# Kernel tuning notes

Hardware: AMD Instinct MI355X
Metric: run time of the kernel (lower is better)

The kernel has to match this reference:

```python
import jax, jax.numpy as jnp
import numpy as np

EMB = 1024
HEADS = 16
HEAD_SZ = EMB // HEADS
EPS = 1e-5


def _layernorm(x, g, b):
    mu = jnp.mean(x, axis=-1, keepdims=True)
    var = jnp.mean(jnp.square(x - mu), axis=-1, keepdims=True)
    return (x - mu) * jax.lax.rsqrt(var + EPS) * g + b


def setup_inputs() -> dict:
    key = jax.random.key(0)
    ks = jax.random.split(key, 12)
    s_in = 1.0 / np.sqrt(EMB)
    s_h = 1.0 / np.sqrt(4 * EMB)
    return {
        "x": jax.random.normal(ks[0], (4, 1024, EMB), jnp.float32),
        # per-head Q/K/V projections stacked: [H, EMB, HEAD_SZ], no bias
        "wq": jax.random.normal(ks[1], (HEADS, EMB, HEAD_SZ), jnp.float32) * s_in,
        "wk": jax.random.normal(ks[2], (HEADS, EMB, HEAD_SZ), jnp.float32) * s_in,
        "wv": jax.random.normal(ks[3], (HEADS, EMB, HEAD_SZ), jnp.float32) * s_in,
        "w_proj": jax.random.normal(ks[4], (EMB, EMB), jnp.float32) * s_in,
        "b_proj": jnp.zeros((EMB,), jnp.float32),
        "w1": jax.random.normal(ks[5], (EMB, 4 * EMB), jnp.float32) * s_in,
        "b1": jnp.zeros((4 * EMB,), jnp.float32),
        "w2": jax.random.normal(ks[6], (4 * EMB, EMB), jnp.float32) * s_h,
        "b2": jnp.zeros((EMB,), jnp.float32),
        "g1": jnp.ones((EMB,), jnp.float32),
        "be1": jnp.zeros((EMB,), jnp.float32),
        "g2": jnp.ones((EMB,), jnp.float32),
        "be2": jnp.zeros((EMB,), jnp.float32),
    }


def reference(x, wq, wk, wv, w_proj, b_proj, w1, b1, w2, b2, g1, be1, g2, be2):
    B, T, C = x.shape
    # --- self-attention (pre-norm) ---
    h = _layernorm(x, g1, be1)
    q = jnp.einsum("btc,hcd->bhtd", h, wq)
    k = jnp.einsum("btc,hcd->bhtd", h, wk)
    v = jnp.einsum("btc,hcd->bhtd", h, wv)
    scale = 1.0 / jnp.sqrt(jnp.asarray(HEAD_SZ, x.dtype))
    scores = jnp.einsum("bhtd,bhsd->bhts", q, k) * scale  # non-causal: SDPA called with no mask
    attn = jax.nn.softmax(scores, axis=-1)
    o = jnp.einsum("bhts,bhsd->bhtd", attn, v)
    o = o.transpose(0, 2, 1, 3).reshape(B, T, C)  # concat heads (same order as torch.cat)
    sa_out = o @ w_proj + b_proj
    x = x + sa_out
    # --- feed-forward; note ln2 applied twice, faithful to source ---
    t = _layernorm(x, g2, be2)
    t = _layernorm(t, g2, be2)
    ff = jax.nn.relu(t @ w1 + b1) @ w2 + b2
    return x + ff
```

## Files before the change

### kernel.cpp

```cpp
#include <hip/hip_runtime.h>
#include <hip/hip_bf16.h>
#include <math.h>
#include <stdint.h>

typedef __bf16 bf16_t;
typedef __bf16 bf16x4 __attribute__((ext_vector_type(4)));
typedef __bf16 bf16x8 __attribute__((ext_vector_type(8)));
typedef float floatx4 __attribute__((ext_vector_type(4)));

#define BM 128
#define BN 128
#define BK 32

__device__ __forceinline__ void gload16(const void* g, void* lds) {
    __builtin_amdgcn_global_load_lds(
        (__attribute__((address_space(1))) void*)(uintptr_t)g,
        (__attribute__((address_space(3))) void*)(uintptr_t)lds,
        16, 0, 0);
}

__global__ void transpose_cast(const float* __restrict__ in, bf16_t* __restrict__ out,
                               int R, int C, long in_z, long out_z)
{
    __shared__ float tile[64][65];
    const int tid = threadIdx.x;
    in  += (long)blockIdx.z * in_z;
    out += (long)blockIdx.z * out_z;
    const int rt = blockIdx.x * 64;
    const int ct = blockIdx.y * 64;
    const int tr = tid >> 4;
    const int tc = (tid & 15) * 4;
#pragma unroll
    for (int rr = 0; rr < 4; rr++) {
        const int r = tr + rr * 16;
        const float4 v = *(const float4*)&in[(long)(rt + r) * C + ct + tc];
        tile[r][tc + 0] = v.x; tile[r][tc + 1] = v.y;
        tile[r][tc + 2] = v.z; tile[r][tc + 3] = v.w;
    }
    __syncthreads();
#pragma unroll
    for (int rr = 0; rr < 4; rr++) {
        const int c = tr + rr * 16;
        bf16x4 o;
        o[0] = (bf16_t)tile[tc + 0][c];
        o[1] = (bf16_t)tile[tc + 1][c];
        o[2] = (bf16_t)tile[tc + 2][c];
        o[3] = (bf16_t)tile[tc + 3][c];
        *(bf16x4*)&out[(long)(ct + c) * R + rt + tc] = o;
    }
}

__global__ void ln_kernel(const float* __restrict__ x, const float* __restrict__ g,
                          const float* __restrict__ b, bf16_t* __restrict__ outb,
                          float* __restrict__ outf)
{
    const int row = blockIdx.x;
    const int tid = threadIdx.x;
    const float4 v = ((const float4*)(x + (long)row * 1024))[tid];
    float s  = v.x + v.y + v.z + v.w;
    float s2 = v.x * v.x + v.y * v.y + v.z * v.z + v.w * v.w;
#pragma unroll
    for (int off = 32; off >= 1; off >>= 1) {
        s  += __shfl_xor(s, off);
        s2 += __shfl_xor(s2, off);
    }
    __shared__ float red[8];
    const int wv = tid >> 6;
    if ((tid & 63) == 0) { red[wv] = s; red[4 + wv] = s2; }
    __syncthreads();
    s  = red[0] + red[1] + red[2] + red[3];
    s2 = red[4] + red[5] + red[6] + red[7];
    const float mu  = s * (1.0f / 1024.0f);
    const float var = fmaxf(s2 * (1.0f / 1024.0f) - mu * mu, 0.0f);
    const float rs  = rsqrtf(var + 1e-5f);
    const float4 gv = ((const float4*)g)[tid];
    const float4 bv = ((const float4*)b)[tid];
    const float y0 = (v.x - mu) * rs * gv.x + bv.x;
    const float y1 = (v.y - mu) * rs * gv.y + bv.y;
    const float y2 = (v.z - mu) * rs * gv.z + bv.z;
    const float y3 = (v.w - mu) * rs * gv.w + bv.w;
    if (outb) {
        bf16x4 o; o[0] = (bf16_t)y0; o[1] = (bf16_t)y1; o[2] = (bf16_t)y2; o[3] = (bf16_t)y3;
        ((bf16x4*)(outb + (long)row * 1024))[tid] = o;
    }
    if (outf) {
        float4 o; o.x = y0; o.y = y1; o.z = y2; o.w = y3;
        ((float4*)(outf + (long)row * 1024))[tid] = o;
    }
}

__global__ void ln2x_kernel(const float* __restrict__ x, const float* __restrict__ g,
                            const float* __restrict__ b, bf16_t* __restrict__ outb)
{
    const int row = blockIdx.x;
    const int tid = threadIdx.x;
    const float4 v = ((const float4*)(x + (long)row * 1024))[tid];
    float s  = v.x + v.y + v.z + v.w;
    float s2 = v.x * v.x + v.y * v.y + v.z * v.z + v.w * v.w;
#pragma unroll
    for (int off = 32; off >= 1; off >>= 1) {
        s  += __shfl_xor(s, off);
        s2 += __shfl_xor(s2, off);
    }
    __shared__ float red[8];
    __shared__ float red2[8];
    const int wv = tid >> 6;
    if ((tid & 63) == 0) { red[wv] = s; red[4 + wv] = s2; }
    __syncthreads();
    s  = red[0] + red[1] + red[2] + red[3];
    s2 = red[4] + red[5] + red[6] + red[7];
    float mu  = s * (1.0f / 1024.0f);
    float var = fmaxf(s2 * (1.0f / 1024.0f) - mu * mu, 0.0f);
    float rs  = rsqrtf(var + 1e-5f);
    const float4 gv = ((const float4*)g)[tid];
    const float4 bv = ((const float4*)b)[tid];
    float y0 = (v.x - mu) * rs * gv.x + bv.x;
    float y1 = (v.y - mu) * rs * gv.y + bv.y;
    float y2 = (v.z - mu) * rs * gv.z + bv.z;
    float y3 = (v.w - mu) * rs * gv.w + bv.w;
    s  = y0 + y1 + y2 + y3;
    s2 = y0 * y0 + y1 * y1 + y2 * y2 + y3 * y3;
#pragma unroll
    for (int off = 32; off >= 1; off >>= 1) {
        s  += __shfl_xor(s, off);
        s2 += __shfl_xor(s2, off);
    }
    if ((tid & 63) == 0) { red2[wv] = s; red2[4 + wv] = s2; }
    __syncthreads();
    s  = red2[0] + red2[1] + red2[2] + red2[3];
    s2 = red2[4] + red2[5] + red2[6] + red2[7];
    mu  = s * (1.0f / 1024.0f);
    var = fmaxf(s2 * (1.0f / 1024.0f) - mu * mu, 0.0f);
    rs  = rsqrtf(var + 1e-5f);
    bf16x4 o;
    o[0] = (bf16_t)((y0 - mu) * rs * gv.x + bv.x);
    o[1] = (bf16_t)((y1 - mu) * rs * gv.y + bv.y);
    o[2] = (bf16_t)((y2 - mu) * rs * gv.z + bv.z);
    o[3] = (bf16_t)((y3 - mu) * rs * gv.w + bv.w);
    ((bf16x4*)(outb + (long)row * 1024))[tid] = o;
}

template<int EPI>
__global__ __launch_bounds__(256, 2)
void gemm_bt(const bf16_t* __restrict__ A, const bf16_t* __restrict__ Bt,
             const int K,
             const float* __restrict__ bias, const float* __restrict__ resid,
             float* __restrict__ outf, bf16_t* __restrict__ outb,
             bf16_t* __restrict__ aux1, bf16_t* __restrict__ aux2,
             const int Nout)
{
    __shared__ __align__(16) bf16_t As[3][BM * BK];
    __shared__ __align__(16) bf16_t Bs[3][BN * BK];
    const int tid  = threadIdx.x;
    const int wave = tid >> 6, lane = tid & 63;
    const int bm = blockIdx.x * BM, bn = blockIdx.y * BN;
    const int wm = (wave >> 1) * 64, wn = (wave & 1) * 64;

    floatx4 acc[4][4];
#pragma unroll
    for (int i = 0; i < 4; i++)
#pragma unroll
        for (int j = 0; j < 4; j++) acc[i][j] = (floatx4){0.f, 0.f, 0.f, 0.f};

    const int srow  = lane >> 2;
    const int sbyte = (lane & 3) * 16;
    const char* gA0 = (const char*)(A  + (size_t)(bm + wave * 32 + srow)      * K) + sbyte;
    const char* gA1 = (const char*)(A  + (size_t)(bm + wave * 32 + 16 + srow) * K) + sbyte;
    const char* gB0 = (const char*)(Bt + (size_t)(bn + wave * 32 + srow)      * K) + sbyte;
    const char* gB1 = (const char*)(Bt + (size_t)(bn + wave * 32 + 16 + srow) * K) + sbyte;
    const int laOff0 = (wave * 32) * 64;
    const int laOff1 = (wave * 32 + 16) * 64;

    const int fr = lane & 15;
    const int fk = (lane >> 4) * 8;

    auto stage = [&](int t, int bu) {
        const size_t kb = (size_t)t * (BK * 2);
        gload16(gA0 + kb, (char*)As[bu] + laOff0);
        gload16(gA1 + kb, (char*)As[bu] + laOff1);
        gload16(gB0 + kb, (char*)Bs[bu] + laOff0);
        gload16(gB1 + kb, (char*)Bs[bu] + laOff1);
    };

    auto compute = [&](int bu) {
        bf16x8 af[4], bfv[4];
#pragma unroll
        for (int i = 0; i < 4; i++) af[i]  = *(const bf16x8*)&As[bu][(wm + i * 16 + fr) * BK + fk];
#pragma unroll
        for (int j = 0; j < 4; j++) bfv[j] = *(const bf16x8*)&Bs[bu][(wn + j * 16 + fr) * BK + fk];
#pragma unroll
        for (int i = 0; i < 4; i++)
#pragma unroll
            for (int j = 0; j < 4; j++)
                acc[i][j] = __builtin_amdgcn_mfma_f32_16x16x32_bf16(af[i], bfv[j], acc[i][j], 0, 0, 0);
    };

    const int NT = K / BK;
    stage(0, 0);
    stage(1, 1);
    int bu = 0;
    for (int t = 0; t < NT - 1; ++t) {
        asm volatile("s_waitcnt vmcnt(4)\n\ts_barrier" ::: "memory");
        if (t + 2 < NT) stage(t + 2, (t + 2) % 3);
        compute(bu);
        bu = (bu + 1) % 3;
    }
    asm volatile("s_waitcnt vmcnt(0)\n\ts_barrier" ::: "memory");
    compute(bu);

    const int er = (lane >> 4) * 4, ec = lane & 15;
#pragma unroll
    for (int i = 0; i < 4; i++) {
#pragma unroll
        for (int j = 0; j < 4; j++) {
            const int col = bn + wn + j * 16 + ec;
#pragma unroll
            for (int r = 0; r < 4; r++) {
                const int row = bm + wm + i * 16 + er + r;
                const float v = acc[i][j][r];
                if (EPI == 0) {
                    const int b = row >> 10, t = row & 1023;
                    if (col < 1024) {
                        const int h = col >> 6, d = col & 63;
                        outb[(size_t)((b * 16 + h) * 1024 + t) * 64 + d] = (bf16_t)v;
                    } else if (col < 2048) {
                        const int c2 = col - 1024, h = c2 >> 6, d = c2 & 63;
                        aux1[(size_t)((b * 16 + h) * 1024 + t) * 64 + d] = (bf16_t)v;
                    } else {
                        const int c2 = col - 2048, h = c2 >> 6, d = c2 & 63;
                        aux2[(size_t)((b * 16 + h) * 64 + d) * 1024 + t] = (bf16_t)v;
                    }
                } else if (EPI == 1 || EPI == 3) {
                    const size_t idx = (size_t)row * Nout + col;
                    outf[idx] = v + bias[col] + resid[idx];
                } else if (EPI == 2) {
                    const size_t idx = (size_t)row * Nout + col;
                    outb[idx] = (bf16_t)fmaxf(v + bias[col], 0.f);
                }
            }
        }
    }
}

__global__ __launch_bounds__(256, 3)
void attn_kernel(const bf16_t* __restrict__ Q, const bf16_t* __restrict__ Kg,
                 const bf16_t* __restrict__ Vt, bf16_t* __restrict__ Og)
{
    __shared__ __align__(16) bf16_t Ks[2][4096];
    __shared__ __align__(16) bf16_t Vs[2][4096];
    __shared__ __align__(16) bf16_t Ps[4][1024];
    const int tid = threadIdx.x, wave = tid >> 6, lane = tid & 63;
    const int bh = blockIdx.y;
    const int b = bh >> 4, h = bh & 15;
    const int q0 = blockIdx.x * 64 + wave * 16;
    const bf16_t* Qb = Q + (size_t)bh * 65536;
    const char* Kb = (const char*)(Kg + (size_t)bh * 65536);
    const char* Vb = (const char*)(Vt + (size_t)bh * 65536);
    const int fr = lane & 15, g = lane >> 4, fk = g * 8;

    const bf16x8 qf0 = *(const bf16x8*)&Qb[(size_t)(q0 + fr) * 64 + fk];
    const bf16x8 qf1 = *(const bf16x8*)&Qb[(size_t)(q0 + fr) * 64 + 32 + fk];

    floatx4 o[4];
#pragma unroll
    for (int dt = 0; dt < 4; dt++) o[dt] = (floatx4){0.f, 0.f, 0.f, 0.f};
    float lsum[4] = {0.f, 0.f, 0.f, 0.f};
    bf16_t* pw = &Ps[wave][0];
    const float sscale = 0.125f * 1.44269504088896f;

    auto stage = [&](int s0, int bu) {
#pragma unroll
        for (int t = 0; t < 2; t++) {
            const int j = wave * 2 + t;
            gload16(Kb + (size_t)(s0 + lane) * 128 + j * 16, &Ks[bu][j * 512]);
            gload16(Vb + (size_t)lane * 2048 + (size_t)s0 * 2 + j * 16, &Vs[bu][j * 512]);
        }
    };

    stage(0, 0);
    int bu = 0;
    for (int it = 0; it < 16; ++it) {
        __syncthreads();
        if (it < 15) stage((it + 1) * 64, bu ^ 1);
        const bf16_t* Kl = Ks[bu];
        const bf16_t* Vl = Vs[bu];

        floatx4 sacc[4];
#pragma unroll
        for (int ss = 0; ss < 4; ss++) sacc[ss] = (floatx4){0.f, 0.f, 0.f, 0.f};
#pragma unroll
        for (int c = 0; c < 2; c++) {
            const int ch = c * 4 + g;
            const bf16x8 qf = (c == 0) ? qf0 : qf1;
#pragma unroll
            for (int ss = 0; ss < 4; ss++) {
                const bf16x8 kf = *(const bf16x8*)&Kl[ch * 512 + (ss * 16 + fr) * 8];
                sacc[ss] = __builtin_amdgcn_mfma_f32_16x16x32_bf16(qf, kf, sacc[ss], 0, 0, 0);
            }
        }
#pragma unroll
        for (int ss = 0; ss < 4; ss++) {
#pragma unroll
            for (int r = 0; r < 4; r++) {
                const float p = __builtin_amdgcn_exp2f(sacc[ss][r] * sscale);
                lsum[r] += p;
                const int q = g * 4 + r;
                pw[(ss * 2 + (fr >> 3)) * 128 + q * 8 + (fr & 7)] = (bf16_t)p;
            }
        }
        asm volatile("s_waitcnt lgkmcnt(0)" ::: "memory");
#pragma unroll
        for (int c = 0; c < 2; c++) {
            const int ch = c * 4 + g;
            const bf16x8 pf = *(const bf16x8*)&pw[ch * 128 + fr * 8];
#pragma unroll
            for (int dt = 0; dt < 4; dt++) {
                const bf16x8 vf = *(const bf16x8*)&Vl[ch * 512 + (dt * 16 + fr) * 8];
                o[dt] = __builtin_amdgcn_mfma_f32_16x16x32_bf16(pf, vf, o[dt], 0, 0, 0);
            }
        }
        asm volatile("" ::: "memory");
        bu ^= 1;
    }
#pragma unroll
    for (int r = 0; r < 4; r++) {
        float l = lsum[r];
        l += __shfl_xor(l, 1);
        l += __shfl_xor(l, 2);
        l += __shfl_xor(l, 4);
        l += __shfl_xor(l, 8);
        lsum[r] = 1.0f / l;
    }
    const int t = q0 + g * 4;
#pragma unroll
    for (int dt = 0; dt < 4; dt++) {
#pragma unroll
        for (int r = 0; r < 4; r++) {
            const size_t idx = ((size_t)(b * 1024 + t + r)) * 1024 + h * 64 + dt * 16 + fr;
            Og[idx] = (bf16_t)(o[dt][r] * lsum[r]);
        }
    }
}

extern "C" void kernel_launch(void* const* d_in, const int* in_sizes, int n_in,
                              void* d_out, int out_size, void* d_ws, size_t ws_size,
                              hipStream_t stream)
{
    const float* x      = (const float*)d_in[0];
    const float* wq     = (const float*)d_in[1];
    const float* wk     = (const float*)d_in[2];
    const float* wv     = (const float*)d_in[3];
    const float* w_proj = (const float*)d_in[4];
    const float* b_proj = (const float*)d_in[5];
    const float* w1     = (const float*)d_in[6];
    const float* b1     = (const float*)d_in[7];
    const float* w2     = (const float*)d_in[8];
    const float* b2     = (const float*)d_in[9];
    const float* g1     = (const float*)d_in[10];
    const float* be1    = (const float*)d_in[11];
    const float* g2     = (const float*)d_in[12];
    const float* be2    = (const float*)d_in[13];
    float* out = (float*)d_out;
    char* ws = (char*)d_ws;

    bf16_t* WQKVT = (bf16_t*)(ws + 0x0000000);
    bf16_t* WPROJT= (bf16_t*)(ws + 0x0600000);
    bf16_t* W1T   = (bf16_t*)(ws + 0x0800000);
    bf16_t* W2T   = (bf16_t*)(ws + 0x1000000);
    bf16_t* HB    = (bf16_t*)(ws + 0x1800000);
    bf16_t* Qb    = (bf16_t*)(ws + 0x2000000);
    bf16_t* Kb    = (bf16_t*)(ws + 0x2800000);
    bf16_t* Vtb   = (bf16_t*)(ws + 0x3000000);
    bf16_t* AO    = (bf16_t*)(ws + 0x3800000);
    float*  X2    = (float*)(ws + 0x4000000);
    bf16_t* TB    = (bf16_t*)(ws + 0x2800000);
    bf16_t* FF1B  = (bf16_t*)(ws + 0x5000000);

    dim3 blk(256);
    transpose_cast<<<dim3(16, 1, 16), blk, 0, stream>>>(wq, WQKVT,             1024, 64,  65536, 65536);
    transpose_cast<<<dim3(16, 1, 16), blk, 0, stream>>>(wk, WQKVT + (1 << 20), 1024, 64,  65536, 65536);
    transpose_cast<<<dim3(16, 1, 16), blk, 0, stream>>>(wv, WQKVT + (2 << 20), 1024, 64,  65536, 65536);
    transpose_cast<<<dim3(16, 16, 1), blk, 0, stream>>>(w_proj, WPROJT, 1024, 1024, 0, 0);
    transpose_cast<<<dim3(16, 64, 1), blk, 0, stream>>>(w1, W1T, 1024, 4096, 0, 0);
    transpose_cast<<<dim3(64, 16, 1), blk, 0, stream>>>(w2, W2T, 4096, 1024, 0, 0);

    ln_kernel<<<4096, blk, 0, stream>>>(x, g1, be1, HB, nullptr);
    gemm_bt<0><<<dim3(32, 24), blk, 0, stream>>>(HB, WQKVT, 1024, nullptr, nullptr,
                                                 nullptr, Qb, Kb, Vtb, 3072);
    attn_kernel<<<dim3(16, 64), blk, 0, stream>>>(Qb, Kb, Vtb, AO);
    gemm_bt<1><<<dim3(32, 8), blk, 0, stream>>>(AO, WPROJT, 1024, b_proj, x,
                                                X2, nullptr, nullptr, nullptr, 1024);
    ln2x_kernel<<<4096, blk, 0, stream>>>(X2, g2, be2, TB);
    gemm_bt<2><<<dim3(32, 32), blk, 0, stream>>>(TB, W1T, 1024, b1, nullptr,
                                                 nullptr, FF1B, nullptr, nullptr, 4096);
    gemm_bt<3><<<dim3(32, 8), blk, 0, stream>>>(FF1B, W2T, 4096, b2, X2,
                                                out, nullptr, nullptr, nullptr, 1024);
}
```

Baseline: 339.4 us.

## Merge weight transposes, add narrow-N GEMM tiles, raise attention occupancy

Folds the six weight transpose-cast launches into one kernel indexed by block id. Templates the GEMM on the N tile width and changes the warp layout so each wave owns 32 rows across the full N tile. The N=1024 projection and FF2 GEMMs now use 64-wide tiles, doubling their grid from 256 to 512 blocks to fill more CUs. Also raises the attention launch-bounds occupancy hint from 3 to 4, which may add register pressure, and the new warp layout gives each wave less operand reuse per LDS read.

```diff
diff --git a/kernel.cpp b/kernel.cpp
--- a/kernel.cpp
+++ b/kernel.cpp
@@ -9,7 +9,6 @@
 typedef float floatx4 __attribute__((ext_vector_type(4)));
 
 #define BM 128
-#define BN 128
 #define BK 32
 
 __device__ __forceinline__ void gload16(const void* g, void* lds) {
@@ -19,21 +18,39 @@
         16, 0, 0);
 }
 
-__global__ void transpose_cast(const float* __restrict__ in, bf16_t* __restrict__ out,
-                               int R, int C, long in_z, long out_z)
-{
+__global__ void transpose_all(const float* __restrict__ wq, const float* __restrict__ wk,
+                              const float* __restrict__ wv, const float* __restrict__ w_proj,
+                              const float* __restrict__ w1, const float* __restrict__ w2,
+                              bf16_t* __restrict__ WQKVT, bf16_t* __restrict__ WPROJT,
+                              bf16_t* __restrict__ W1T, bf16_t* __restrict__ W2T)
+{
+    const int idx = blockIdx.x;
+    const float* in; bf16_t* out; int R, C, rt, ct;
+    if (idx < 768) {
+        const int z = idx >> 8;
+        const int hd = (idx >> 4) & 15;
+        rt = idx & 15; ct = 0; R = 1024; C = 64;
+        in  = (z == 0 ? wq : z == 1 ? wk : wv) + hd * 65536;
+        out = WQKVT + z * (1 << 20) + hd * 65536;
+    } else if (idx < 1024) {
+        const int t = idx - 768; rt = t & 15; ct = t >> 4; R = 1024; C = 1024;
+        in = w_proj; out = WPROJT;
+    } else if (idx < 2048) {
+        const int t = idx - 1024; rt = t & 15; ct = t >> 4; R = 1024; C = 4096;
+        in = w1; out = W1T;
+    } else {
+        const int t = idx - 2048; rt = t & 63; ct = t >> 6; R = 4096; C = 1024;
+        in = w2; out = W2T;
+    }
     __shared__ float tile[64][65];
     const int tid = threadIdx.x;
-    in  += (long)blockIdx.z * in_z;
-    out += (long)blockIdx.z * out_z;
-    const int rt = blockIdx.x * 64;
-    const int ct = blockIdx.y * 64;
+    const int r0 = rt * 64, c0 = ct * 64;
     const int tr = tid >> 4;
     const int tc = (tid & 15) * 4;
 #pragma unroll
     for (int rr = 0; rr < 4; rr++) {
         const int r = tr + rr * 16;
-        const float4 v = *(const float4*)&in[(long)(rt + r) * C + ct + tc];
+        const float4 v = *(const float4*)&in[(long)(r0 + r) * C + c0 + tc];
         tile[r][tc + 0] = v.x; tile[r][tc + 1] = v.y;
         tile[r][tc + 2] = v.z; tile[r][tc + 3] = v.w;
     }
@@ -46,13 +63,12 @@
         o[1] = (bf16_t)tile[tc + 1][c];
         o[2] = (bf16_t)tile[tc + 2][c];
         o[3] = (bf16_t)tile[tc + 3][c];
-        *(bf16x4*)&out[(long)(ct + c) * R + rt + tc] = o;
+        *(bf16x4*)&out[(long)(c0 + c) * R + r0 + tc] = o;
     }
 }
 
 __global__ void ln_kernel(const float* __restrict__ x, const float* __restrict__ g,
-                          const float* __restrict__ b, bf16_t* __restrict__ outb,
-                          float* __restrict__ outf)
+                          const float* __restrict__ b, bf16_t* __restrict__ outb)
 {
     const int row = blockIdx.x;
     const int tid = threadIdx.x;
@@ -75,18 +91,12 @@
     const float rs  = rsqrtf(var + 1e-5f);
     const float4 gv = ((const float4*)g)[tid];
     const float4 bv = ((const float4*)b)[tid];
-    const float y0 = (v.x - mu) * rs * gv.x + bv.x;
-    const float y1 = (v.y - mu) * rs * gv.y + bv.y;
-    const float y2 = (v.z - mu) * rs * gv.z + bv.z;
-    const float y3 = (v.w - mu) * rs * gv.w + bv.w;
-    if (outb) {
-        bf16x4 o; o[0] = (bf16_t)y0; o[1] = (bf16_t)y1; o[2] = (bf16_t)y2; o[3] = (bf16_t)y3;
-        ((bf16x4*)(outb + (long)row * 1024))[tid] = o;
-    }
-    if (outf) {
-        float4 o; o.x = y0; o.y = y1; o.z = y2; o.w = y3;
-        ((float4*)(outf + (long)row * 1024))[tid] = o;
-    }
+    bf16x4 o;
+    o[0] = (bf16_t)((v.x - mu) * rs * gv.x + bv.x);
+    o[1] = (bf16_t)((v.y - mu) * rs * gv.y + bv.y);
+    o[2] = (bf16_t)((v.z - mu) * rs * gv.z + bv.z);
+    o[3] = (bf16_t)((v.w - mu) * rs * gv.w + bv.w);
+    ((bf16x4*)(outb + (long)row * 1024))[tid] = o;
 }
 
 __global__ void ln2x_kernel(const float* __restrict__ x, const float* __restrict__ g,
@@ -140,7 +150,7 @@
     ((bf16x4*)(outb + (long)row * 1024))[tid] = o;
 }
 
-template<int EPI>
+template<int EPI, int BNt>
 __global__ __launch_bounds__(256, 2)
 void gemm_bt(const bf16_t* __restrict__ A, const bf16_t* __restrict__ Bt,
              const int K,
@@ -149,27 +159,34 @@
              bf16_t* __restrict__ aux1, bf16_t* __restrict__ aux2,
              const int Nout)
 {
+    constexpr int NFRAG = BNt / 16;
     __shared__ __align__(16) bf16_t As[3][BM * BK];
-    __shared__ __align__(16) bf16_t Bs[3][BN * BK];
+    __shared__ __align__(16) bf16_t Bs[3][BNt * BK];
     const int tid  = threadIdx.x;
     const int wave = tid >> 6, lane = tid & 63;
-    const int bm = blockIdx.x * BM, bn = blockIdx.y * BN;
-    const int wm = (wave >> 1) * 64, wn = (wave & 1) * 64;
-
-    floatx4 acc[4][4];
-#pragma unroll
-    for (int i = 0; i < 4; i++)
-#pragma unroll
-        for (int j = 0; j < 4; j++) acc[i][j] = (floatx4){0.f, 0.f, 0.f, 0.f};
+    const int bm = blockIdx.x * BM, bn = blockIdx.y * BNt;
+
+    floatx4 acc[2][NFRAG];
+#pragma unroll
+    for (int i = 0; i < 2; i++)
+#pragma unroll
+        for (int j = 0; j < NFRAG; j++) acc[i][j] = (floatx4){0.f, 0.f, 0.f, 0.f};
 
     const int srow  = lane >> 2;
     const int sbyte = (lane & 3) * 16;
-    const char* gA0 = (const char*)(A  + (size_t)(bm + wave * 32 + srow)      * K) + sbyte;
-    const char* gA1 = (const char*)(A  + (size_t)(bm + wave * 32 + 16 + srow) * K) + sbyte;
-    const char* gB0 = (const char*)(Bt + (size_t)(bn + wave * 32 + srow)      * K) + sbyte;
-    const char* gB1 = (const char*)(Bt + (size_t)(bn + wave * 32 + 16 + srow) * K) + sbyte;
+    const char* gA0 = (const char*)(A + (size_t)(bm + wave * 32 + srow)      * K) + sbyte;
+    const char* gA1 = (const char*)(A + (size_t)(bm + wave * 32 + 16 + srow) * K) + sbyte;
+    const char* gB0;
+    const char* gB1 = nullptr;
+    if (BNt == 128) {
+        gB0 = (const char*)(Bt + (size_t)(bn + wave * 32 + srow)      * K) + sbyte;
+        gB1 = (const char*)(Bt + (size_t)(bn + wave * 32 + 16 + srow) * K) + sbyte;
+    } else {
+        gB0 = (const char*)(Bt + (size_t)(bn + wave * 16 + srow) * K) + sbyte;
+    }
     const int laOff0 = (wave * 32) * 64;
     const int laOff1 = (wave * 32 + 16) * 64;
+    const int lbOff0 = (BNt == 128) ? laOff0 : (wave * 16) * 64;
 
     const int fr = lane & 15;
     const int fk = (lane >> 4) * 8;
@@ -178,20 +195,22 @@
         const size_t kb = (size_t)t * (BK * 2);
         gload16(gA0 + kb, (char*)As[bu] + laOff0);
         gload16(gA1 + kb, (char*)As[bu] + laOff1);
-        gload16(gB0 + kb, (char*)Bs[bu] + laOff0);
-        gload16(gB1 + kb, (char*)Bs[bu] + laOff1);
+        gload16(gB0 + kb, (char*)Bs[bu] + lbOff0);
+        if (BNt == 128) gload16(gB1 + kb, (char*)Bs[bu] + laOff1);
     };
 
     auto compute = [&](int bu) {
-        bf16x8 af[4], bfv[4];
-#pragma unroll
-        for (int i = 0; i < 4; i++) af[i]  = *(const bf16x8*)&As[bu][(wm + i * 16 + fr) * BK + fk];
-#pragma unroll
-        for (int j = 0; j < 4; j++) bfv[j] = *(const bf16x8*)&Bs[bu][(wn + j * 16 + fr) * BK + fk];
-#pragma unroll
-        for (int i = 0; i < 4; i++)
-#pragma unroll
-            for (int j = 0; j < 4; j++)
+        bf16x8 af[2], bfv[NFRAG];
+#pragma unroll
+        for (int i = 0; i < 2; i++)
+            af[i] = *(const bf16x8*)&As[bu][(wave * 32 + i * 16 + fr) * BK + fk];
+#pragma unroll
+        for (int j = 0; j < NFRAG; j++)
+            bfv[j] = *(const bf16x8*)&Bs[bu][(j * 16 + fr) * BK + fk];
+#pragma unroll
+        for (int i = 0; i < 2; i++)
+#pragma unroll
+            for (int j = 0; j < NFRAG; j++)
                 acc[i][j] = __builtin_amdgcn_mfma_f32_16x16x32_bf16(af[i], bfv[j], acc[i][j], 0, 0, 0);
     };
 
@@ -200,7 +219,8 @@
     stage(1, 1);
     int bu = 0;
     for (int t = 0; t < NT - 1; ++t) {
-        asm volatile("s_waitcnt vmcnt(4)\n\ts_barrier" ::: "memory");
+        if (BNt == 128) asm volatile("s_waitcnt vmcnt(4)\n\ts_barrier" ::: "memory");
+        else            asm volatile("s_waitcnt vmcnt(3)\n\ts_barrier" ::: "memory");
         if (t + 2 < NT) stage(t + 2, (t + 2) % 3);
         compute(bu);
         bu = (bu + 1) % 3;
@@ -210,13 +230,13 @@
 
     const int er = (lane >> 4) * 4, ec = lane & 15;
 #pragma unroll
-    for (int i = 0; i < 4; i++) {
-#pragma unroll
-        for (int j = 0; j < 4; j++) {
-            const int col = bn + wn + j * 16 + ec;
+    for (int i = 0; i < 2; i++) {
+#pragma unroll
+        for (int j = 0; j < NFRAG; j++) {
+            const int col = bn + j * 16 + ec;
 #pragma unroll
             for (int r = 0; r < 4; r++) {
-                const int row = bm + wm + i * 16 + er + r;
+                const int row = bm + wave * 32 + i * 16 + er + r;
                 const float v = acc[i][j][r];
                 if (EPI == 0) {
                     const int b = row >> 10, t = row & 1023;
@@ -242,7 +262,7 @@
     }
 }
 
-__global__ __launch_bounds__(256, 3)
+__global__ __launch_bounds__(256, 4)
 void attn_kernel(const bf16_t* __restrict__ Q, const bf16_t* __restrict__ Kg,
                  const bf16_t* __restrict__ Vt, bf16_t* __restrict__ Og)
 {
@@ -377,22 +397,17 @@
     bf16_t* FF1B  = (bf16_t*)(ws + 0x5000000);
 
     dim3 blk(256);
-    transpose_cast<<<dim3(16, 1, 16), blk, 0, stream>>>(wq, WQKVT,             1024, 64,  65536, 65536);
-    transpose_cast<<<dim3(16, 1, 16), blk, 0, stream>>>(wk, WQKVT + (1 << 20), 1024, 64,  65536, 65536);
-    transpose_cast<<<dim3(16, 1, 16), blk, 0, stream>>>(wv, WQKVT + (2 << 20), 1024, 64,  65536, 65536);
-    transpose_cast<<<dim3(16, 16, 1), blk, 0, stream>>>(w_proj, WPROJT, 1024, 1024, 0, 0);
-    transpose_cast<<<dim3(16, 64, 1), blk, 0, stream>>>(w1, W1T, 1024, 4096, 0, 0);
-    transpose_cast<<<dim3(64, 16, 1), blk, 0, stream>>>(w2, W2T, 4096, 1024, 0, 0);
-
-    ln_kernel<<<4096, blk, 0, stream>>>(x, g1, be1, HB, nullptr);
-    gemm_bt<0><<<dim3(32, 24), blk, 0, stream>>>(HB, WQKVT, 1024, nullptr, nullptr,
-                                                 nullptr, Qb, Kb, Vtb, 3072);
+    transpose_all<<<3072, blk, 0, stream>>>(wq, wk, wv, w_proj, w1, w2,
+                                            WQKVT, WPROJT, W1T, W2T);
+    ln_kernel<<<4096, blk, 0, stream>>>(x, g1, be1, HB);
+    gemm_bt<0, 128><<<dim3(32, 24), blk, 0, stream>>>(HB, WQKVT, 1024, nullptr, nullptr,
+                                                      nullptr, Qb, Kb, Vtb, 3072);
     attn_kernel<<<dim3(16, 64), blk, 0, stream>>>(Qb, Kb, Vtb, AO);
-    gemm_bt<1><<<dim3(32, 8), blk, 0, stream>>>(AO, WPROJT, 1024, b_proj, x,
-                                                X2, nullptr, nullptr, nullptr, 1024);
+    gemm_bt<1, 64><<<dim3(32, 16), blk, 0, stream>>>(AO, WPROJT, 1024, b_proj, x,
+                                                     X2, nullptr, nullptr, nullptr, 1024);
     ln2x_kernel<<<4096, blk, 0, stream>>>(X2, g2, be2, TB);
-    gemm_bt<2><<<dim3(32, 32), blk, 0, stream>>>(TB, W1T, 1024, b1, nullptr,
-                                                 nullptr, FF1B, nullptr, nullptr, 4096);
-    gemm_bt<3><<<dim3(32, 8), blk, 0, stream>>>(FF1B, W2T, 4096, b2, X2,
-                                                out, nullptr, nullptr, nullptr, 1024);
-}
+    gemm_bt<2, 128><<<dim3(32, 32), blk, 0, stream>>>(TB, W1T, 1024, b1, nullptr,
+                                                      nullptr, FF1B, nullptr, nullptr, 4096);
+    gemm_bt<3, 64><<<dim3(32, 16), blk, 0, stream>>>(FF1B, W2T, 4096, b2, X2,
+                                                     out, nullptr, nullptr, nullptr, 1024);
+}
```

Measured after the change: 324.6 us. -4.4%, faster.
